# Kernel tuning notes

Measured on AMD Instinct MI355X. Metric: run time of the kernel, lower is better.

The kernel has to match this reference:

```python
import jax, jax.numpy as jnp
import numpy as np

MARGIN = 5.0
NUM_CLASSES = 21


def setup_inputs() -> dict:
    key = jax.random.key(0)
    k1, k2, k3 = jax.random.split(key, 3)
    B, D, C = 65536, 512, NUM_CLASSES
    features = jax.random.normal(k1, (B, D), dtype=jnp.float32)
    centers = jax.random.normal(k2, (C, D), dtype=jnp.float32)
    labels = jax.random.randint(k3, (B,), 0, C, dtype=jnp.int64)
    return {"features": features, "centers": centers, "labels": labels}


def reference(features, centers, labels):
    # Halved squared euclidean distances, batch x num_classes, via the
    # ||f||^2 + ||c||^2 - 2 f.c expansion (avoids a B x C x D intermediate).
    f2 = jnp.sum(features * features, axis=1, keepdims=True)      # (B, 1)
    c2 = jnp.sum(centers * centers, axis=1)[None, :]              # (1, C)
    d = 0.5 * (f2 + c2 - 2.0 * (features @ centers.T))            # (B, C)

    B = features.shape[0]
    pos = d[jnp.arange(B), labels]                                 # dist to own center
    same = labels[:, None] == jnp.arange(NUM_CLASSES)[None, :]     # (B, C)
    neg = jnp.min(jnp.where(same, jnp.inf, d), axis=1)             # nearest other center
    loss = jnp.mean(jax.nn.relu(pos + MARGIN - neg))
    return loss
```

## Files before the change

kernel.cpp:

```cpp
#include <hip/hip_runtime.h>
#include <float.h>

#define DIM      512
#define NCLS     21
#define MARGIN_V 5.0f
#define NWAVES   4
#define DSLICE   (DIM / NWAVES)
#define RPL      4
#define ROWS_PB  (64 * RPL)
#define CHFLT    8
#define NCHUNK   (DSLICE / CHFLT)
#define CLDSF    (NCLS * DIM)
#define SST      (RPL * NCLS + 1)
#define LDSF     (2 * 64 * SST)

__global__ __launch_bounds__(64)
void center_norm_kernel(const float* __restrict__ centers,
                        float* __restrict__ halfc2) {
    const int c = blockIdx.x;
    const int t = threadIdx.x;
    float s = 0.f;
#pragma unroll
    for (int i = 0; i < DIM / 64; ++i) {
        float v = centers[c * DIM + i * 64 + t];
        s = fmaf(v, v, s);
    }
#pragma unroll
    for (int off = 32; off > 0; off >>= 1)
        s += __shfl_down(s, off, 64);
    if (t == 0) halfc2[c] = 0.5f * s;
}

__global__ __launch_bounds__(256)
void tcl_main_kernel(const float* __restrict__ feat,
                     const float* __restrict__ centers,
                     const int* __restrict__ labels,
                     const float* __restrict__ halfc2,
                     float* __restrict__ out) {
    __shared__ float lds_f[LDSF];

    const int tid  = threadIdx.x;
    const int w    = __builtin_amdgcn_readfirstlane(tid >> 6);
    const int t    = tid & 63;
    const int row0 = blockIdx.x * ROWS_PB;

    int labv[RPL];
    if (w == 0) {
#pragma unroll
        for (int r = 0; r < RPL; ++r) labv[r] = labels[row0 + t + r * 64];
    }

    float acc[RPL][NCLS];
#pragma unroll
    for (int r = 0; r < RPL; ++r)
#pragma unroll
        for (int c = 0; c < NCLS; ++c) acc[r][c] = 0.f;

    const float4* f4p = reinterpret_cast<const float4*>(feat);
    size_t rb[RPL];
#pragma unroll
    for (int r = 0; r < RPL; ++r)
        rb[r] = (size_t)(row0 + t + r * 64) * (DIM / 4) + (size_t)w * (DSLICE / 4);

    float4* l4 = reinterpret_cast<float4*>(lds_f);
    {
        const float4* c4 = reinterpret_cast<const float4*>(centers);
#pragma unroll
        for (int i = 0; i < (CLDSF / 4 + 255) / 256; ++i) {
            int idx = i * 256 + tid;
            if (idx < CLDSF / 4) l4[idx] = c4[idx];
        }
    }
    __syncthreads();

    const float4* cl = l4 + w * (DSLICE / 4);

    auto LOADC = [&](float4 (&dst)[RPL][2], int kk) {
#pragma unroll
        for (int r = 0; r < RPL; ++r)
#pragma unroll
            for (int j = 0; j < 2; ++j)
                dst[r][j] = f4p[rb[r] + kk * 2 + j];
    };
    auto COMPUTE = [&](const float4 (&f)[RPL][2], int kk) {
#pragma unroll
        for (int q = 0; q < 2; ++q) {
            const int fq = kk * 2 + q;
#pragma unroll
            for (int ch = 0; ch < 3; ++ch) {
                float4 cv[7];
#pragma unroll
                for (int k7 = 0; k7 < 7; ++k7)
                    cv[k7] = cl[(ch * 7 + k7) * (DIM / 4) + fq];
#pragma unroll
                for (int k7 = 0; k7 < 7; ++k7) {
                    const int c = ch * 7 + k7;
#pragma unroll
                    for (int r = 0; r < RPL; ++r) {
                        acc[r][c] = fmaf(f[r][q].x, cv[k7].x,
                                     fmaf(f[r][q].y, cv[k7].y,
                                      fmaf(f[r][q].z, cv[k7].z,
                                       fmaf(f[r][q].w, cv[k7].w, acc[r][c]))));
                    }
                }
            }
        }
    };

    float4 fA[RPL][2], fB[RPL][2];
    LOADC(fA, 0);
#pragma unroll 1
    for (int k = 0; k < NCHUNK - 2; k += 2) {
        LOADC(fB, k + 1);
        COMPUTE(fA, k);
        LOADC(fA, k + 2);
        COMPUTE(fB, k + 1);
    }
    LOADC(fB, NCHUNK - 1);
    COMPUTE(fA, NCHUNK - 2);
    COMPUTE(fB, NCHUNK - 1);

    float* scratch = lds_f;
    __syncthreads();
    if (w >= 2) {
        float* p = &scratch[((w - 2) * 64 + t) * SST];
#pragma unroll
        for (int r = 0; r < RPL; ++r)
#pragma unroll
            for (int c = 0; c < NCLS; ++c) p[r * NCLS + c] = acc[r][c];
    }
    __syncthreads();
    if (w < 2) {
        const float* p = &scratch[(w * 64 + t) * SST];
#pragma unroll
        for (int r = 0; r < RPL; ++r)
#pragma unroll
            for (int c = 0; c < NCLS; ++c) acc[r][c] += p[r * NCLS + c];
    }
    __syncthreads();
    if (w == 1) {
        float* p = &scratch[t * SST];
#pragma unroll
        for (int r = 0; r < RPL; ++r)
#pragma unroll
            for (int c = 0; c < NCLS; ++c) p[r * NCLS + c] = acc[r][c];
    }
    __syncthreads();
    if (w == 0) {
        const float* p = &scratch[t * SST];
        float vsum = 0.f;
#pragma unroll
        for (int r = 0; r < RPL; ++r) {
            const int lab = labv[r];
            float pos = 0.f, neg = FLT_MAX;
#pragma unroll
            for (int c = 0; c < NCLS; ++c) {
                float e = halfc2[c] - (acc[r][c] + p[r * NCLS + c]);
                pos = (c == lab) ? e : pos;
                neg = (c == lab) ? neg : fminf(neg, e);
            }
            vsum += fmaxf(pos + MARGIN_V - neg, 0.f);
        }
#pragma unroll
        for (int off = 32; off > 0; off >>= 1)
            vsum += __shfl_down(vsum, off, 64);
        if (t == 0) atomicAdd(out, vsum * (1.0f / 65536.f));
    }
}

extern "C" void kernel_launch(void* const* d_in, const int* in_sizes, int n_in,
                              void* d_out, int out_size, void* d_ws, size_t ws_size,
                              hipStream_t stream) {
    const float* feat    = (const float*)d_in[0];
    const float* centers = (const float*)d_in[1];
    const int*   labels  = (const int*)d_in[2];
    float* out    = (float*)d_out;
    float* halfc2 = (float*)d_ws;

    hipMemsetAsync(d_out, 0, (size_t)out_size * sizeof(float), stream);
    center_norm_kernel<<<NCLS, 64, 0, stream>>>(centers, halfc2);

    const int nblocks = 65536 / ROWS_PB;
    tcl_main_kernel<<<nblocks, 256, 0, stream>>>(feat, centers, labels, halfc2, out);
}
```

Before: 217.1 us.

## Transpose centers in LDS, halve rows per lane, overlap first feature load

Centers are stored in LDS transposed so each float4 group of all 21 classes sits contiguously. All lanes then read the same addresses as broadcasts instead of strided rows. Rows per lane drop from 4 to 2, doubling the block count and lowering register pressure. The first feature chunk is issued before the center staging, and sched_barriers pin the load/compute interleave. The trade-off is less feature reuse per center load, and the reduction scratch now shares the transposed-center LDS buffer, whose size has changed.

```diff
diff --git a/kernel.cpp b/kernel.cpp
--- a/kernel.cpp
+++ b/kernel.cpp
@@ -6,13 +6,14 @@
 #define MARGIN_V 5.0f
 #define NWAVES   4
 #define DSLICE   (DIM / NWAVES)
-#define RPL      4
+#define RPL      2
 #define ROWS_PB  (64 * RPL)
 #define CHFLT    8
 #define NCHUNK   (DSLICE / CHFLT)
-#define CLDSF    (NCLS * DIM)
+#define NF4      (DIM / 4)
+#define CT_F4    (NF4 * NCLS)
 #define SST      (RPL * NCLS + 1)
-#define LDSF     (2 * 64 * SST)
+#define LDSF     (CT_F4 * 4)
 
 __global__ __launch_bounds__(64)
 void center_norm_kernel(const float* __restrict__ centers,
@@ -57,23 +58,11 @@
         for (int c = 0; c < NCLS; ++c) acc[r][c] = 0.f;
 
     const float4* f4p = reinterpret_cast<const float4*>(feat);
+    const int g0 = w * (DSLICE / 4);
     size_t rb[RPL];
 #pragma unroll
     for (int r = 0; r < RPL; ++r)
-        rb[r] = (size_t)(row0 + t + r * 64) * (DIM / 4) + (size_t)w * (DSLICE / 4);
-
-    float4* l4 = reinterpret_cast<float4*>(lds_f);
-    {
-        const float4* c4 = reinterpret_cast<const float4*>(centers);
-#pragma unroll
-        for (int i = 0; i < (CLDSF / 4 + 255) / 256; ++i) {
-            int idx = i * 256 + tid;
-            if (idx < CLDSF / 4) l4[idx] = c4[idx];
-        }
-    }
-    __syncthreads();
-
-    const float4* cl = l4 + w * (DSLICE / 4);
+        rb[r] = (size_t)(row0 + t + r * 64) * NF4 + g0;
 
     auto LOADC = [&](float4 (&dst)[RPL][2], int kk) {
 #pragma unroll
@@ -82,41 +71,59 @@
             for (int j = 0; j < 2; ++j)
                 dst[r][j] = f4p[rb[r] + kk * 2 + j];
     };
+
+    float4 fA[RPL][2], fB[RPL][2];
+    LOADC(fA, 0);
+    __builtin_amdgcn_sched_barrier(0);
+
+    float4* ct = reinterpret_cast<float4*>(lds_f);
+    {
+        const float4* c4 = reinterpret_cast<const float4*>(centers);
+#pragma unroll
+        for (int i = 0; i < (CT_F4 + 255) / 256; ++i) {
+            int idx = i * 256 + tid;
+            if (idx < CT_F4) {
+                float4 v = c4[idx];
+                int c = idx >> 7;
+                int g = idx & (NF4 - 1);
+                ct[g * NCLS + c] = v;
+            }
+        }
+    }
+    __syncthreads();
+
     auto COMPUTE = [&](const float4 (&f)[RPL][2], int kk) {
 #pragma unroll
         for (int q = 0; q < 2; ++q) {
-            const int fq = kk * 2 + q;
+            const int gq = g0 + kk * 2 + q;
+            const float4* cbase = &ct[gq * NCLS];
+            float4 cv[NCLS];
 #pragma unroll
-            for (int ch = 0; ch < 3; ++ch) {
-                float4 cv[7];
+            for (int c = 0; c < NCLS; ++c) cv[c] = cbase[c];
 #pragma unroll
-                for (int k7 = 0; k7 < 7; ++k7)
-                    cv[k7] = cl[(ch * 7 + k7) * (DIM / 4) + fq];
+            for (int c = 0; c < NCLS; ++c) {
 #pragma unroll
-                for (int k7 = 0; k7 < 7; ++k7) {
-                    const int c = ch * 7 + k7;
-#pragma unroll
-                    for (int r = 0; r < RPL; ++r) {
-                        acc[r][c] = fmaf(f[r][q].x, cv[k7].x,
-                                     fmaf(f[r][q].y, cv[k7].y,
-                                      fmaf(f[r][q].z, cv[k7].z,
-                                       fmaf(f[r][q].w, cv[k7].w, acc[r][c]))));
-                    }
+                for (int r = 0; r < RPL; ++r) {
+                    acc[r][c] = fmaf(f[r][q].x, cv[c].x,
+                                 fmaf(f[r][q].y, cv[c].y,
+                                  fmaf(f[r][q].z, cv[c].z,
+                                   fmaf(f[r][q].w, cv[c].w, acc[r][c]))));
                 }
             }
         }
     };
 
-    float4 fA[RPL][2], fB[RPL][2];
-    LOADC(fA, 0);
 #pragma unroll 1
     for (int k = 0; k < NCHUNK - 2; k += 2) {
         LOADC(fB, k + 1);
+        __builtin_amdgcn_sched_barrier(0);
         COMPUTE(fA, k);
         LOADC(fA, k + 2);
+        __builtin_amdgcn_sched_barrier(0);
         COMPUTE(fB, k + 1);
     }
     LOADC(fB, NCHUNK - 1);
+    __builtin_amdgcn_sched_barrier(0);
     COMPUTE(fA, NCHUNK - 2);
     COMPUTE(fB, NCHUNK - 1);
 
```

Measured after the change: 211.1 us. -2.8%, faster.
